# Optimization experiments

Hardware: AMD Instinct MI355X
Metric: run time of the kernel (lower is better)

Reference implementation:

```python
import jax, jax.numpy as jnp
import numpy as np

B, N, C = 2, 768, 64
PH, AH = 32, 32  # pos_mlp / attn_mlp hidden dims
NEG = -1e9


def setup_inputs() -> dict:
    key = jax.random.key(0)
    ks = jax.random.split(key, 20)
    g = lambda k, shape, fan_in: jax.random.normal(k, shape, jnp.float32) / np.sqrt(fan_in)
    return {
        "coords": jax.random.normal(ks[0], (B, N, 3), jnp.float32),
        "mask": jax.random.bernoulli(ks[1], 0.9, (B, N)),
        # coord_embed: Dense(3->C, relu), Dense(C->C)
        "ce_w1": g(ks[2], (3, C), 3), "ce_b1": jnp.zeros((C,), jnp.float32),
        "ce_w2": g(ks[3], (C, C), C), "ce_b2": jnp.zeros((C,), jnp.float32),
        # q/k/v projections (no bias)
        "wq": g(ks[4], (C, C), C), "wk": g(ks[5], (C, C), C), "wv": g(ks[6], (C, C), C),
        # pos_mlp: Dense(3->PH, relu), Dense(PH->C)
        "pm_w1": g(ks[7], (3, PH), 3), "pm_b1": jnp.zeros((PH,), jnp.float32),
        "pm_w2": g(ks[8], (PH, C), PH), "pm_b2": jnp.zeros((C,), jnp.float32),
        # attn_mlp: Dense(C->AH, relu), Dense(AH->C)
        "am_w1": g(ks[9], (C, AH), C), "am_b1": jnp.zeros((AH,), jnp.float32),
        "am_w2": g(ks[10], (AH, C), AH), "am_b2": jnp.zeros((C,), jnp.float32),
        # linear_out: Dense(C->C) with bias
        "out_w": g(ks[11], (C, C), C), "out_b": jnp.zeros((C,), jnp.float32),
    }


def reference(coords, mask, ce_w1, ce_b1, ce_w2, ce_b2, wq, wk, wv,
              pm_w1, pm_b1, pm_w2, pm_b2, am_w1, am_b1, am_w2, am_b2,
              out_w, out_b):
    # coord embedding: (B,N,3) -> (B,N,C)
    x = jax.nn.relu(coords @ ce_w1 + ce_b1) @ ce_w2 + ce_b2
    q = x @ wq
    k = x @ wk
    v = x @ wv
    # pairwise relative positions: (B,N,N,3)
    rel_pos = coords[:, :, None, :] - coords[:, None, :, :]
    # positional encoding MLP: (B,N,N,C)
    pos_enc = jax.nn.relu(rel_pos @ pm_w1 + pm_b1) @ pm_w2 + pm_b2
    # vector attention logits: q_i - k_j + pos_enc_ij, then elementwise MLP
    attn = q[:, :, None, :] - k[:, None, :, :] + pos_enc  # (B,N,N,C)
    attn = jax.nn.relu(attn @ am_w1 + am_b1) @ am_w2 + am_b2
    # mask invalid keys (axis 2), per-channel softmax over keys
    attn = jnp.where(mask[:, None, :, None], attn, NEG)
    attn = jax.nn.softmax(attn, axis=2)
    # aggregate: sum_j attn_ij * (v_j + pos_enc_ij) -> (B,N,C)
    output = jnp.sum(attn * (v[:, None, :, :] + pos_enc), axis=2)
    return output @ out_w + out_b + x
```

## Files before the change

### kernel.cpp

```cpp
#include <hip/hip_runtime.h>
#include <hip/hip_bf16.h>

#define NB 2
#define NN 768
#define NC 64
#define NPH 32
#define NAH 32
#define NEGV -1e9f
#define LOG2E 1.4426950408889634f

typedef __attribute__((ext_vector_type(8))) short bf16x8;
typedef __attribute__((ext_vector_type(4))) float f32x4;

__device__ __forceinline__ short f2bf(float f) {
    unsigned u = __builtin_bit_cast(unsigned, f);
    u = (u + 0x7FFFu + ((u >> 16) & 1u)) >> 16;
    return (short)u;
}

__device__ __forceinline__ unsigned cvt_pk_bf16(float lo, float hi) {
    unsigned r;
    asm("v_cvt_pk_bf16_f32 %0, %1, %2" : "=v"(r) : "v"(lo), "v"(hi));
    return r;
}

__device__ __forceinline__ float bflo(unsigned u) { return __builtin_bit_cast(float, u << 16); }
__device__ __forceinline__ float bfhi(unsigned u) { return __builtin_bit_cast(float, u & 0xffff0000u); }

__device__ __forceinline__ void gload_lds16(const void* g, void* l) {
    __builtin_amdgcn_global_load_lds(
        (const __attribute__((address_space(1))) unsigned int*)g,
        (__attribute__((address_space(3))) unsigned int*)l,
        16, 0, 0);
}

__global__ __launch_bounds__(64)
void embed_kernel(const float* __restrict__ coords,
                  const float* __restrict__ ce_w1, const float* __restrict__ ce_b1,
                  const float* __restrict__ ce_w2, const float* __restrict__ ce_b2,
                  const float* __restrict__ wq, const float* __restrict__ wk,
                  const float* __restrict__ wv,
                  const float* __restrict__ am_w1, const float* __restrict__ am_b1,
                  const float* __restrict__ pm_w1,
                  const float* __restrict__ pm_w2, const float* __restrict__ pm_b2,
                  const float* __restrict__ am_w2,
                  const void* __restrict__ maskp,
                  float* __restrict__ x, short* __restrict__ vth,
                  float* __restrict__ qc, float* __restrict__ kw1,
                  float* __restrict__ hcf,
                  unsigned long long* __restrict__ maskw,
                  short* __restrict__ w12T, short* __restrict__ peT,
                  short* __restrict__ a2P)
{
    const int row = blockIdx.x;
    const int c = threadIdx.x;
    __shared__ float h1[NC];
    __shared__ float xs[NC];
    __shared__ float qs[NC];
    __shared__ float ks[NC];
    __shared__ int cnt;
    if (c == 0) cnt = 0;
    float p0 = coords[row*3+0], p1 = coords[row*3+1], p2 = coords[row*3+2];
    if (c < NPH) {
        float hcv = fmaf(p0, pm_w1[c], fmaf(p1, pm_w1[NPH+c], p2 * pm_w1[2*NPH+c]));
        hcf[row*NPH + c] = hcv;
    }
    float h = fmaf(p0, ce_w1[c], fmaf(p1, ce_w1[NC+c], fmaf(p2, ce_w1[2*NC+c], ce_b1[c])));
    h1[c] = fmaxf(h, 0.f);
    __syncthreads();
    float acc = ce_b2[c];
    for (int d = 0; d < NC; ++d) acc = fmaf(h1[d], ce_w2[d*NC+c], acc);
    xs[c] = acc;
    x[row*NC+c] = acc;
    __syncthreads();
    float aq = 0.f, ak = 0.f, av = 0.f;
    for (int d = 0; d < NC; ++d) {
        float xv = xs[d];
        aq = fmaf(xv, wq[d*NC+c], aq);
        ak = fmaf(xv, wk[d*NC+c], ak);
        av = fmaf(xv, wv[d*NC+c], av);
    }
    qs[c] = aq; ks[c] = ak;
    {
        int bb = row / NN, nn = row - bb*NN;
        int tile = nn >> 4, jj = nn & 15;
        int lp = ((jj >> 2) << 4) | (c & 15);
        int kp = ((c >> 4) << 2) | (jj & 3);
        vth[((size_t)bb*48 + tile)*1024 + lp*16 + kp] = f2bf(av + pm_b2[c]);
    }
    __syncthreads();
    if (c < NAH) {
        float a2 = am_b1[c];
        for (int d = 0; d < NC; ++d) a2 = fmaf(qs[d] + pm_b2[d], am_w1[d*NAH+c], a2);
        qc[row*NAH+c] = a2;
    } else {
        int hh = c - NAH;
        float a2 = 0.f;
        for (int d = 0; d < NC; ++d) a2 = fmaf(ks[d], am_w1[d*NAH+hh], a2);
        kw1[row*NAH+hh] = a2;
    }

    if (row == 0) {
        const unsigned char* mB = (const unsigned char*)maskp;
        const int* mI = (const int*)maskp;
        int local = 0;
        for (int t = c; t < NB*NN; t += NC) local += (mB[t] == 1) ? 1 : 0;
        atomicAdd(&cnt, local);
        __syncthreads();
        int isByte = (cnt > 800);
        if (c < 24) {
            unsigned long long bits = 0ull;
            for (int e = 0; e < 64; ++e) {
                int j = c*64 + e;
                int mv = isByte ? (int)mB[j] : mI[j];
                bits |= (unsigned long long)((mv != 0) ? 1 : 0) << e;
            }
            maskw[c] = bits;
        }
    }
    if (row >= 1 && row <= 8) {
        int ri = row - 1;
        #pragma unroll
        for (int t = 0; t < 2; ++t) {
            int o = ri*128 + c*2 + t;
            int c2 = o >> 5, p = o & 31;
            float a2 = 0.f;
            for (int d = 0; d < NC; ++d) a2 = fmaf(pm_w2[p*NC+d], am_w1[d*NAH+c2], a2);
            w12T[o] = f2bf(a2);
        }
    }
    if (row >= 9 && row <= 16) {
        int ri = row - 9;
        #pragma unroll
        for (int t = 0; t < 4; ++t) {
            int o = ri*256 + c*4 + t;
            int cc = o >> 5, hh = o & 31;
            peT[o] = f2bf(pm_w2[hh*NC + cc]);
        }
    }
    if (row >= 17 && row <= 24) {
        int ri = row - 17;
        #pragma unroll
        for (int t = 0; t < 4; ++t) {
            int o = ri*256 + c*4 + t;
            int cc = o >> 5, s = o & 31;
            int e = s & 7, kg = s >> 3;
            int hh = ((e >> 2) << 4) + kg*4 + (e & 3);
            a2P[o] = f2bf(am_w2[hh*NC + cc] * LOG2E);
        }
    }
}

__global__ __launch_bounds__(256, 3)
void attn_kernel(const float* __restrict__ pm_w1, const float* __restrict__ pm_b1,
                 const float* __restrict__ out_w, const float* __restrict__ out_b,
                 const float* __restrict__ xg, const float* __restrict__ coords,
                 const short* __restrict__ vth,
                 const float* __restrict__ qcg, const float* __restrict__ kw1g,
                 const float* __restrict__ hcfg,
                 const unsigned long long* __restrict__ maskw,
                 const short* __restrict__ w12T, const short* __restrict__ peT,
                 const short* __restrict__ a2P,
                 float* __restrict__ out)
{
    const int tid  = threadIdx.x;
    const int wv   = tid >> 6;
    const int lane = tid & 63;
    const int cl   = lane & 15;
    const int kgp  = lane >> 4;

    const int bi0 = blockIdx.x * 2;
    const int b   = bi0 / NN;

    __shared__ __align__(16) char stage[4][2][4096];
    __shared__ __align__(16) float sW1j[NPH][4];
    __shared__ float comb[2][2][4][NC];
    __shared__ float agg[2][NC];

    if (tid < NPH) {
        sW1j[tid][0] = pm_w1[tid];
        sW1j[tid][1] = pm_w1[NPH + tid];
        sW1j[tid][2] = pm_w1[2*NPH + tid];
        sW1j[tid][3] = 0.f;
    }

    bf16x8 bPE[4], bW12[2], bA2[4];
    #pragma unroll
    for (int nt = 0; nt < 4; ++nt) bPE[nt] = *(const bf16x8*)(peT + (nt*16+cl)*NPH + kgp*8);
    #pragma unroll
    for (int ht = 0; ht < 2; ++ht) bW12[ht] = *(const bf16x8*)(w12T + (ht*16+cl)*NPH + kgp*8);
    #pragma unroll
    for (int nt = 0; nt < 4; ++nt) bA2[nt] = *(const bf16x8*)(a2P + (nt*16+cl)*NPH + kgp*8);

    f32x4 qcC[2][2], hciA[2][2];
    {
        f32x4 b1a = *(const f32x4*)(pm_b1 + kgp*8);
        f32x4 b1b = *(const f32x4*)(pm_b1 + kgp*8 + 4);
        #pragma unroll
        for (int g = 0; g < 2; ++g) {
            #pragma unroll
            for (int ht = 0; ht < 2; ++ht)
                qcC[g][ht] = *(const f32x4*)(qcg + (size_t)(bi0+g)*NAH + ht*16 + kgp*4);
            f32x4 h0 = *(const f32x4*)(hcfg + (size_t)(bi0+g)*NPH + kgp*8);
            f32x4 h1 = *(const f32x4*)(hcfg + (size_t)(bi0+g)*NPH + kgp*8 + 4);
            hciA[g][0] = h0 + b1a;
            hciA[g][1] = h1 + b1b;
        }
    }

    const int maskBase = b * NN;
    const float* cjp  = coords + (size_t)(maskBase + wv*16 + cl) * 3;
    const float* krow = kw1g + (size_t)(maskBase + wv*16 + cl) * NAH + kgp*4;
    const short* vvp  = vth + ((size_t)b*48 + wv)*1024 + (size_t)lane*16;
    const unsigned long long* mwp = maskw + b*12;
    const int shft = wv*16 + kgp*4;

    float l_[2][4], ac_[2][4];
    #pragma unroll
    for (int g = 0; g < 2; ++g)
        #pragma unroll
        for (int nt = 0; nt < 4; ++nt) { l_[g][nt] = 0.f; ac_[g][nt] = 0.f; }
    const f32x4 z4 = {0.f, 0.f, 0.f, 0.f};

    __syncthreads();

    auto stage_tile = [&](int t, int buf) {
        char* base = &stage[wv][buf][0];
        const float* kr = krow + (size_t)t*2048;
        const short* vs = vvp  + (size_t)t*4096;
        gload_lds16(kr,      base);
        gload_lds16(kr + 16, base + 1024);
        gload_lds16(vs,      base + 2048);
        gload_lds16(vs + 8,  base + 3072);
    };

    stage_tile(0, 0);

    for (int p = 0; p < 12; ++p) {
        if (p < 11) {
            stage_tile(p + 1, (p + 1) & 1);
            asm volatile("s_waitcnt vmcnt(4)" ::: "memory");
        } else {
            asm volatile("s_waitcnt vmcnt(0)" ::: "memory");
        }

        const char* base = &stage[wv][p & 1][0];
        f32x4 kv0  = *(const f32x4*)(base + (size_t)lane*16);
        f32x4 kv1  = *(const f32x4*)(base + 1024 + (size_t)lane*16);
        bf16x8 vv0 = *(const bf16x8*)(base + 2048 + (size_t)lane*16);
        bf16x8 vv1 = *(const bf16x8*)(base + 3072 + (size_t)lane*16);
        float cj0 = cjp[p*192 + 0], cj1 = cjp[p*192 + 1], cj2 = cjp[p*192 + 2];
        unsigned bits4 = (unsigned)(mwp[p] >> shft) & 0xFu;

        float hj[8];
        #pragma unroll
        for (int e = 0; e < 8; ++e) {
            const f32x4 w = *(const f32x4*)&sW1j[kgp*8+e][0];
            hj[e] = fmaf(cj0, w[0], fmaf(cj1, w[1], cj2 * w[2]));
        }

        const unsigned* vq0 = (const unsigned*)&vv0;
        const unsigned* vq1 = (const unsigned*)&vv1;
        f32x4 vA[4];
        vA[0][0]=bflo(vq0[0]); vA[0][1]=bfhi(vq0[0]); vA[0][2]=bflo(vq0[1]); vA[0][3]=bfhi(vq0[1]);
        vA[1][0]=bflo(vq0[2]); vA[1][1]=bfhi(vq0[2]); vA[1][2]=bflo(vq0[3]); vA[1][3]=bfhi(vq0[3]);
        vA[2][0]=bflo(vq1[0]); vA[2][1]=bfhi(vq1[0]); vA[2][2]=bflo(vq1[1]); vA[2][3]=bfhi(vq1[1]);
        vA[3][0]=bflo(vq1[2]); vA[3][1]=bfhi(vq1[2]); vA[3][2]=bflo(vq1[3]); vA[3][3]=bfhi(vq1[3]);

        #pragma unroll
        for (int g = 0; g < 2; ++g) {
            float hv[8];
            #pragma unroll
            for (int e = 0; e < 4; ++e) {
                hv[e]   = fmaxf(hciA[g][0][e] - hj[e],   0.f);
                hv[4+e] = fmaxf(hciA[g][1][e] - hj[4+e], 0.f);
            }
            union { bf16x8 h8; unsigned u[4]; } aHP;
            #pragma unroll
            for (int p2 = 0; p2 < 4; ++p2) aHP.u[p2] = cvt_pk_bf16(hv[2*p2], hv[2*p2+1]);

            f32x4 pe[4];
            #pragma unroll
            for (int nt = 0; nt < 4; ++nt)
                pe[nt] = __builtin_amdgcn_mfma_f32_16x16x32_bf16(aHP.h8, bPE[nt], vA[nt], 0, 0, 0);

            f32x4 hT[2];
            #pragma unroll
            for (int ht = 0; ht < 2; ++ht)
                hT[ht] = __builtin_amdgcn_mfma_f32_16x16x32_bf16(bW12[ht], aHP.h8, qcC[g][ht], 0, 0, 0);

            float f8[8];
            #pragma unroll
            for (int r = 0; r < 4; ++r) {
                f8[r]   = fmaxf(hT[0][r] - kv0[r], 0.f);
                f8[4+r] = fmaxf(hT[1][r] - kv1[r], 0.f);
            }
            union { bf16x8 h8; unsigned u[4]; } aH;
            #pragma unroll
            for (int p2 = 0; p2 < 4; ++p2) aH.u[p2] = cvt_pk_bf16(f8[2*p2], f8[2*p2+1]);

            #pragma unroll
            for (int nt = 0; nt < 4; ++nt) {
                f32x4 atl = __builtin_amdgcn_mfma_f32_16x16x32_bf16(aH.h8, bA2[nt], z4, 0, 0, 0);
                #pragma unroll
                for (int r = 0; r < 4; ++r) {
                    float a0 = (bits4 & (1u << r)) ? atl[r] : NEGV;
                    float pp = __builtin_amdgcn_exp2f(a0);
                    l_[g][nt] += pp;
                    ac_[g][nt] = fmaf(pp, pe[nt][r], ac_[g][nt]);
                }
            }
        }
    }

    #pragma unroll
    for (int st = 16; st <= 32; st <<= 1) {
        #pragma unroll
        for (int g = 0; g < 2; ++g)
            #pragma unroll
            for (int nt = 0; nt < 4; ++nt) {
                l_[g][nt]  += __shfl_xor(l_[g][nt], st);
                ac_[g][nt] += __shfl_xor(ac_[g][nt], st);
            }
    }
    if (lane < 16) {
        #pragma unroll
        for (int g = 0; g < 2; ++g)
            #pragma unroll
            for (int nt = 0; nt < 4; ++nt) {
                comb[0][g][wv][nt*16+lane] = l_[g][nt];
                comb[1][g][wv][nt*16+lane] = ac_[g][nt];
            }
    }
    __syncthreads();

    if (tid < 128) {
        int g = tid >> 6, c = tid & 63;
        float lt = 0.f, at2 = 0.f;
        #pragma unroll
        for (int w = 0; w < 4; ++w) { lt += comb[0][g][w][c]; at2 += comb[1][g][w][c]; }
        agg[g][c] = at2 / lt;
    }
    __syncthreads();

    if (tid < 128) {
        int g = tid >> 6, c = tid & 63;
        int bi2 = bi0 + g;
        float o = out_b[c] + xg[(size_t)bi2*NC + c];
        for (int d = 0; d < NC; ++d) o = fmaf(agg[g][d], out_w[d*NC + c], o);
        out[(size_t)bi2*NC + c] = o;
    }
}

extern "C" void kernel_launch(void* const* d_in, const int* in_sizes, int n_in,
                              void* d_out, int out_size, void* d_ws, size_t ws_size,
                              hipStream_t stream) {
    const float* coords = (const float*)d_in[0];
    const void*  maskp  = d_in[1];
    const float* ce_w1  = (const float*)d_in[2];
    const float* ce_b1  = (const float*)d_in[3];
    const float* ce_w2  = (const float*)d_in[4];
    const float* ce_b2  = (const float*)d_in[5];
    const float* wq     = (const float*)d_in[6];
    const float* wk     = (const float*)d_in[7];
    const float* wvw    = (const float*)d_in[8];
    const float* pm_w1  = (const float*)d_in[9];
    const float* pm_b1  = (const float*)d_in[10];
    const float* pm_w2  = (const float*)d_in[11];
    const float* pm_b2  = (const float*)d_in[12];
    const float* am_w1  = (const float*)d_in[13];
    const float* am_b1  = (const float*)d_in[14];
    const float* am_w2  = (const float*)d_in[15];
    const float* out_w  = (const float*)d_in[17];
    const float* out_b  = (const float*)d_in[18];

    char* ws = (char*)d_ws;
    unsigned long long* maskw = (unsigned long long*)ws;
    short* w12T = (short*)(ws + 256);
    short* peT  = (short*)(ws + 4096);
    short* a2P  = (short*)(ws + 8192);
    float* x    = (float*)(ws + 16384);
    short* vth  = (short*)(x + (size_t)NB*NN*NC);
    float* qc   = x + 2*(size_t)NB*NN*NC;
    float* kw1  = qc + (size_t)NB*NN*NAH;
    float* hcf  = kw1 + (size_t)NB*NN*NAH;

    embed_kernel<<<NB*NN, 64, 0, stream>>>(coords, ce_w1, ce_b1, ce_w2, ce_b2,
                                           wq, wk, wvw, am_w1, am_b1, pm_w1, pm_w2, pm_b2, am_w2,
                                           maskp, x, vth, qc, kw1, hcf, maskw, w12T, peT, a2P);
    attn_kernel<<<NB*NN/2, 256, 0, stream>>>(pm_w1, pm_b1, out_w, out_b,
                                             x, coords, vth, qc, kw1, hcf,
                                             maskw, w12T, peT, a2P,
                                             (float*)d_out);
}
```

Measured before the change: 48.41 us.

## Stage precomputed key hidden features via LDS and fold mask into MFMA accumulator

The attention kernel no longer recomputes each key's pos_mlp first-layer projection from coords and pm_w1 inside the loop. It streams the precomputed hcf rows through the existing async global-to-LDS double buffer, extending each stage and raising the vmcnt wait count. The key mask is folded into the final MFMA's accumulator init as 0/-1e9 instead of a per-element select, and the comb/agg scratch now reuses the stage buffer behind an extra barrier. The tradeoff is more LDS per block (48KB) and more global traffic per tile in exchange for fewer VALU ops and scalar coord loads.

```diff
diff --git a/kernel.cpp b/kernel.cpp
--- a/kernel.cpp
+++ b/kernel.cpp
@@ -152,9 +152,9 @@
 }
 
 __global__ __launch_bounds__(256, 3)
-void attn_kernel(const float* __restrict__ pm_w1, const float* __restrict__ pm_b1,
+void attn_kernel(const float* __restrict__ pm_b1,
                  const float* __restrict__ out_w, const float* __restrict__ out_b,
-                 const float* __restrict__ xg, const float* __restrict__ coords,
+                 const float* __restrict__ xg,
                  const short* __restrict__ vth,
                  const float* __restrict__ qcg, const float* __restrict__ kw1g,
                  const float* __restrict__ hcfg,
@@ -172,17 +172,9 @@
     const int bi0 = blockIdx.x * 2;
     const int b   = bi0 / NN;
 
-    __shared__ __align__(16) char stage[4][2][4096];
-    __shared__ __align__(16) float sW1j[NPH][4];
-    __shared__ float comb[2][2][4][NC];
-    __shared__ float agg[2][NC];
-
-    if (tid < NPH) {
-        sW1j[tid][0] = pm_w1[tid];
-        sW1j[tid][1] = pm_w1[NPH + tid];
-        sW1j[tid][2] = pm_w1[2*NPH + tid];
-        sW1j[tid][3] = 0.f;
-    }
+    __shared__ __align__(16) char stage[4][2][6144];
+    float* combp = (float*)&stage[0][0][0];
+    float* aggp  = combp + 1024;
 
     bf16x8 bPE[4], bW12[2], bA2[4];
     #pragma unroll
@@ -209,9 +201,9 @@
     }
 
     const int maskBase = b * NN;
-    const float* cjp  = coords + (size_t)(maskBase + wv*16 + cl) * 3;
     const float* krow = kw1g + (size_t)(maskBase + wv*16 + cl) * NAH + kgp*4;
     const short* vvp  = vth + ((size_t)b*48 + wv)*1024 + (size_t)lane*16;
+    const float* hjr  = hcfg + (size_t)(maskBase + wv*16 + cl) * NPH + kgp*8;
     const unsigned long long* mwp = maskw + b*12;
     const int shft = wv*16 + kgp*4;
 
@@ -220,18 +212,18 @@
     for (int g = 0; g < 2; ++g)
         #pragma unroll
         for (int nt = 0; nt < 4; ++nt) { l_[g][nt] = 0.f; ac_[g][nt] = 0.f; }
-    const f32x4 z4 = {0.f, 0.f, 0.f, 0.f};
-
-    __syncthreads();
 
     auto stage_tile = [&](int t, int buf) {
         char* base = &stage[wv][buf][0];
         const float* kr = krow + (size_t)t*2048;
         const short* vs = vvp  + (size_t)t*4096;
+        const float* hr = hjr  + (size_t)t*2048;
         gload_lds16(kr,      base);
         gload_lds16(kr + 16, base + 1024);
         gload_lds16(vs,      base + 2048);
         gload_lds16(vs + 8,  base + 3072);
+        gload_lds16(hr,      base + 4096);
+        gload_lds16(hr + 4,  base + 5120);
     };
 
     stage_tile(0, 0);
@@ -239,7 +231,7 @@
     for (int p = 0; p < 12; ++p) {
         if (p < 11) {
             stage_tile(p + 1, (p + 1) & 1);
-            asm volatile("s_waitcnt vmcnt(4)" ::: "memory");
+            asm volatile("s_waitcnt vmcnt(6)" ::: "memory");
         } else {
             asm volatile("s_waitcnt vmcnt(0)" ::: "memory");
         }
@@ -249,15 +241,13 @@
         f32x4 kv1  = *(const f32x4*)(base + 1024 + (size_t)lane*16);
         bf16x8 vv0 = *(const bf16x8*)(base + 2048 + (size_t)lane*16);
         bf16x8 vv1 = *(const bf16x8*)(base + 3072 + (size_t)lane*16);
-        float cj0 = cjp[p*192 + 0], cj1 = cjp[p*192 + 1], cj2 = cjp[p*192 + 2];
+        f32x4 hj0  = *(const f32x4*)(base + 4096 + (size_t)lane*16);
+        f32x4 hj1  = *(const f32x4*)(base + 5120 + (size_t)lane*16);
         unsigned bits4 = (unsigned)(mwp[p] >> shft) & 0xFu;
 
-        float hj[8];
-        #pragma unroll
-        for (int e = 0; e < 8; ++e) {
-            const f32x4 w = *(const f32x4*)&sW1j[kgp*8+e][0];
-            hj[e] = fmaf(cj0, w[0], fmaf(cj1, w[1], cj2 * w[2]));
-        }
+        f32x4 maskC;
+        #pragma unroll
+        for (int r = 0; r < 4; ++r) maskC[r] = (bits4 & (1u << r)) ? 0.f : NEGV;
 
         const unsigned* vq0 = (const unsigned*)&vv0;
         const unsigned* vq1 = (const unsigned*)&vv1;
@@ -272,8 +262,8 @@
             float hv[8];
             #pragma unroll
             for (int e = 0; e < 4; ++e) {
-                hv[e]   = fmaxf(hciA[g][0][e] - hj[e],   0.f);
-                hv[4+e] = fmaxf(hciA[g][1][e] - hj[4+e], 0.f);
+                hv[e]   = fmaxf(hciA[g][0][e] - hj0[e], 0.f);
+                hv[4+e] = fmaxf(hciA[g][1][e] - hj1[e], 0.f);
             }
             union { bf16x8 h8; unsigned u[4]; } aHP;
             #pragma unroll
@@ -301,11 +291,10 @@
 
             #pragma unroll
             for (int nt = 0; nt < 4; ++nt) {
-                f32x4 atl = __builtin_amdgcn_mfma_f32_16x16x32_bf16(aH.h8, bA2[nt], z4, 0, 0, 0);
+                f32x4 atl = __builtin_amdgcn_mfma_f32_16x16x32_bf16(aH.h8, bA2[nt], maskC, 0, 0, 0);
                 #pragma unroll
                 for (int r = 0; r < 4; ++r) {
-                    float a0 = (bits4 & (1u << r)) ? atl[r] : NEGV;
-                    float pp = __builtin_amdgcn_exp2f(a0);
+                    float pp = __builtin_amdgcn_exp2f(atl[r]);
                     l_[g][nt] += pp;
                     ac_[g][nt] = fmaf(pp, pe[nt][r], ac_[g][nt]);
                 }
@@ -323,13 +312,16 @@
                 ac_[g][nt] += __shfl_xor(ac_[g][nt], st);
             }
     }
+
+    __syncthreads();
+
     if (lane < 16) {
         #pragma unroll
         for (int g = 0; g < 2; ++g)
             #pragma unroll
             for (int nt = 0; nt < 4; ++nt) {
-                comb[0][g][wv][nt*16+lane] = l_[g][nt];
-                comb[1][g][wv][nt*16+lane] = ac_[g][nt];
+                combp[((0*2+g)*4 + wv)*NC + nt*16+lane] = l_[g][nt];
+                combp[((1*2+g)*4 + wv)*NC + nt*16+lane] = ac_[g][nt];
             }
     }
     __syncthreads();
@@ -338,8 +330,11 @@
         int g = tid >> 6, c = tid & 63;
         float lt = 0.f, at2 = 0.f;
         #pragma unroll
-        for (int w = 0; w < 4; ++w) { lt += comb[0][g][w][c]; at2 += comb[1][g][w][c]; }
-        agg[g][c] = at2 / lt;
+        for (int w = 0; w < 4; ++w) {
+            lt  += combp[((0*2+g)*4 + w)*NC + c];
+            at2 += combp[((1*2+g)*4 + w)*NC + c];
+        }
+        aggp[g*NC + c] = at2 / lt;
     }
     __syncthreads();
 
@@ -347,7 +342,7 @@
         int g = tid >> 6, c = tid & 63;
         int bi2 = bi0 + g;
         float o = out_b[c] + xg[(size_t)bi2*NC + c];
-        for (int d = 0; d < NC; ++d) o = fmaf(agg[g][d], out_w[d*NC + c], o);
+        for (int d = 0; d < NC; ++d) o = fmaf(aggp[g*NC + d], out_w[d*NC + c], o);
         out[(size_t)bi2*NC + c] = o;
     }
 }
@@ -388,8 +383,8 @@
     embed_kernel<<<NB*NN, 64, 0, stream>>>(coords, ce_w1, ce_b1, ce_w2, ce_b2,
                                            wq, wk, wvw, am_w1, am_b1, pm_w1, pm_w2, pm_b2, am_w2,
                                            maskp, x, vth, qc, kw1, hcf, maskw, w12T, peT, a2P);
-    attn_kernel<<<NB*NN/2, 256, 0, stream>>>(pm_w1, pm_b1, out_w, out_b,
-                                             x, coords, vth, qc, kw1, hcf,
+    attn_kernel<<<NB*NN/2, 256, 0, stream>>>(pm_b1, out_w, out_b,
+                                             x, vth, qc, kw1, hcf,
                                              maskw, w12T, peT, a2P,
                                              (float*)d_out);
 }
```

After: 45.57 us, median of 2. -5.9%, faster.
